# Kernel tuning notes

Measured on AMD Instinct MI355X. Metric: run time of the kernel, lower is better.

## Reference

```python
import jax, jax.numpy as jnp
import numpy as np

B, M, D = 2048, 40, 64          # batch, num fields, embedding dim
HIDDEN = [128, 128, 128]        # CIN layer sizes


def setup_inputs() -> dict:
    key = jax.random.key(0)
    kx, k0, k1, k2 = jax.random.split(key, 4)
    x = jax.random.normal(kx, (B, M, D), dtype=jnp.float32)
    # torch.rand -> uniform [0, 1)
    W0 = jax.random.uniform(k0, (M, M, HIDDEN[0]), dtype=jnp.float32)
    W1 = jax.random.uniform(k1, (M, HIDDEN[0], HIDDEN[1]), dtype=jnp.float32)
    W2 = jax.random.uniform(k2, (M, HIDDEN[1], HIDDEN[2]), dtype=jnp.float32)
    return {"x": x, "W0": W0, "W1": W1, "W2": W2}


def _cin_forward(x, Ws):
    # x: [b, m, d]. Each layer k:
    #   x_next[b, l, d] = sum_{m, h} x0[b, m, d] * x_k[b, h, d] * W_k[m, h, l]
    # which equals the torch 'bil,bjl->bjil' outer product followed by
    # 'bijk,ijl->bkl' + transpose, but expressed as one fused contraction
    # (opt_einsum picks a path avoiding the worst intermediate).
    ps = []
    xk = x  # [b, H_k, d], H_0 = m
    for W in Ws:
        x_next = jnp.einsum('bmd,bhd,mhl->bld', x, xk, W)  # [b, L_k, d]
        ps.append(jnp.sum(x_next, axis=2))                  # [b, L_k]
        xk = x_next
    return jnp.concatenate(ps, axis=1)                      # [b, sum(L_k)]


def reference(x, W0, W1, W2):
    return _cin_forward(x, (W0, W1, W2))
```

## Files before the change

### kernel.cpp

```cpp
#include <hip/hip_runtime.h>
#include <hip/hip_bf16.h>
#include <cstdint>

#define BATCH 2048
#define MF    40
#define DDIM  64
#define LDIM  128
#define ROWS  (BATCH * DDIM)

typedef __attribute__((ext_vector_type(4)))  short    short4_t;
typedef __attribute__((ext_vector_type(8)))  short    short8;
typedef __attribute__((ext_vector_type(8)))  __bf16   bf16x8;
typedef __attribute__((ext_vector_type(2)))  float    floatx2;
typedef __attribute__((ext_vector_type(16))) float    floatx16;

__device__ __forceinline__ unsigned short f32_to_bf16(float f) {
    union { float f; uint32_t u; } v; v.f = f;
    uint32_t u = v.u;
    uint32_t r = (u + 0x7fffu + ((u >> 16) & 1u)) >> 16;
    return (unsigned short)r;
}

__device__ __forceinline__ void barrier_raw() {
    asm volatile("s_barrier" ::: "memory");
}
__device__ __forceinline__ void lgkmwait0() {
    asm volatile("s_waitcnt lgkmcnt(0)" ::: "memory");
}
template <int N> __device__ __forceinline__ void vmwait() {
    if constexpr (N == 0)  asm volatile("s_waitcnt vmcnt(0)"  ::: "memory");
    if constexpr (N == 4)  asm volatile("s_waitcnt vmcnt(4)"  ::: "memory");
    if constexpr (N == 6)  asm volatile("s_waitcnt vmcnt(6)"  ::: "memory");
    if constexpr (N == 10) asm volatile("s_waitcnt vmcnt(10)" ::: "memory");
}

__global__ void k_wprep_all(const float* __restrict__ W0, const float* __restrict__ W1,
                            const float* __restrict__ W2,
                            unsigned short* __restrict__ W0t,
                            unsigned short* __restrict__ W1t,
                            unsigned short* __restrict__ W2t) {
    int bi = blockIdx.x;
    const float* W; unsigned short* Wt; int KK, H;
    if (bi < 640)       { W = W0; Wt = W0t; KK = 4; H = 40; }
    else if (bi < 1920) { bi -= 640;  W = W1; Wt = W1t; KK = 8; H = 128; }
    else                { bi -= 1920; W = W2; Wt = W2t; KK = 8; H = 128; }
    int lane = threadIdx.x;
    int cb = bi & 3;
    int mkk = bi >> 2;
    int kk = mkk % KK, m = mkk / KK;
    int l = cb * 32 + (lane & 31);
    int hbase = kk * 16 + (lane >> 5) * 8;
    unsigned short o[8];
#pragma unroll
    for (int j = 0; j < 8; ++j) {
        int h = hbase + j;
        float v = (h < H) ? W[((size_t)m * H + h) * LDIM + l] : 0.f;
        o[j] = f32_to_bf16(v);
    }
    *(short8*)(Wt + (((size_t)(m * KK + kk) * 4 + cb) * 64 + lane) * 8) = *(const short8*)o;
}

template <int KK>
__device__ __forceinline__ void layer_loop(
    const unsigned short* __restrict__ Wt,
    const float* __restrict__ x, int b,
    int lane, int hf, int r31, int cbg0, int cbg1,
    unsigned short* slabf,
    bf16x8 (&xk)[2][8], floatx16 (&acc)[2][2])
{
    constexpr int UPM  = KK / 4;
    constexpr int NU   = MF * UPM;
    constexpr int GATE = (KK == 8) ? 10 : 6;

    auto stage = [&](int uu) {
        int u = uu < NU ? uu : NU - 1;
        const unsigned short* src = Wt + (size_t)u * 8192;
        const int tid = threadIdx.x;
#pragma unroll
        for (int it = 0; it < 4; ++it) {
            int c = it * 256 + tid;
            __builtin_amdgcn_global_load_lds(
                (const __attribute__((address_space(1))) uint32_t*)(src + (size_t)c * 8),
                (__attribute__((address_space(3))) uint32_t*)(&slabf[(size_t)(u & 3) * 8192 + (size_t)c * 8]),
                16, 0, 0);
        }
    };
    auto ldfrag = [&](int u, int frag, int cb) {
        return __builtin_bit_cast(bf16x8, *(const short8*)(
            &slabf[(size_t)(u & 3) * 8192 + ((size_t)(frag * 4 + cb) * 64 + lane) * 8]));
    };

    acc[0][0] = floatx16{}; acc[0][1] = floatx16{};
    acc[1][0] = floatx16{}; acc[1][1] = floatx16{};

    vmwait<0>();
    stage(0); stage(1); stage(2);
    vmwait<4>();
    barrier_raw();

    bf16x8 bbuf[2][2];
#pragma unroll
    for (int p = 0; p < 2; ++p) {
        bbuf[p][0] = ldfrag(0, p, cbg0);
        bbuf[p][1] = ldfrag(0, p, cbg1);
    }

    float s0v = 0.f, s1v = 0.f;

#pragma unroll 1
    for (int m = 0; m < MF; ++m) {
        floatx16 P[2][2] = {};
#pragma unroll
        for (int kk = 0; kk < KK; ++kk) {
            if (kk % 4 == 0) {
                barrier_raw();
                asm volatile("s_setprio 1");
                if (kk == 0) {
                    const float* sp = x + ((size_t)b * MF + m) * DDIM + r31;
                    s0v = sp[0];
                    s1v = sp[32];
                }
                stage(m * UPM + kk / 4 + 3);
            }
            const int slot = kk & 1;
            P[0][0] = __builtin_amdgcn_mfma_f32_32x32x16_bf16(bbuf[slot][0], xk[0][kk], P[0][0], 0, 0, 0);
            P[1][0] = __builtin_amdgcn_mfma_f32_32x32x16_bf16(bbuf[slot][0], xk[1][kk], P[1][0], 0, 0, 0);
            P[0][1] = __builtin_amdgcn_mfma_f32_32x32x16_bf16(bbuf[slot][1], xk[0][kk], P[0][1], 0, 0, 0);
            P[1][1] = __builtin_amdgcn_mfma_f32_32x32x16_bf16(bbuf[slot][1], xk[1][kk], P[1][1], 0, 0, 0);
            {
                const int j  = kk + 2;
                int mm = m + ((j >= KK) ? 1 : 0);
                if (mm > MF - 1) mm = MF - 1;
                const int jj = (j >= KK) ? (j - KK) : j;
                const int u  = mm * UPM + jj / 4;
                bbuf[slot][0] = ldfrag(u, jj % 4, cbg0);
                bbuf[slot][1] = ldfrag(u, jj % 4, cbg1);
            }
            if (kk % 4 == 3) vmwait<GATE>();
        }
        asm volatile("s_setprio 0");
#pragma unroll
        for (int t = 0; t < 2; ++t) {
            const float sv = (t == 0) ? s0v : s1v;
            floatx2 s2 = {sv, sv};
#pragma unroll
            for (int cbp = 0; cbp < 2; ++cbp) {
                floatx2*       A = (floatx2*)&acc[t][cbp];
                const floatx2* Q = (const floatx2*)&P[t][cbp];
#pragma unroll
                for (int i = 0; i < 8; ++i) A[i] += s2 * Q[i];
            }
        }
    }
}

__global__ __launch_bounds__(256, 2) void k_cin(
    const float* __restrict__ x,
    const unsigned short* __restrict__ W0t,
    const unsigned short* __restrict__ W1t,
    const unsigned short* __restrict__ W2t,
    float* __restrict__ out)
{
    __shared__ unsigned short slab[4][8192];
    unsigned short* slabf = &slab[0][0];

    const int tid  = threadIdx.x;
    const int lane = tid & 63, wave = tid >> 6;
    const int hf   = lane >> 5, r31 = lane & 31;
    const int rowhalf = wave >> 1, colhalf = wave & 1;
    const int b = blockIdx.x * 2 + rowhalf;
    const int cbg0 = colhalf * 2, cbg1 = colhalf * 2 + 1;

    bf16x8   xk[2][8];
    floatx16 acc[2][2];

    auto write_ps = [&](int OFF) {
#pragma unroll
        for (int cbp = 0; cbp < 2; ++cbp) {
#pragma unroll
            for (int j = 0; j < 16; ++j) {
                float v = acc[0][cbp][j] + acc[1][cbp][j];
                v += __shfl_xor(v, 16);
                v += __shfl_xor(v, 8);
                v += __shfl_xor(v, 4);
                v += __shfl_xor(v, 2);
                v += __shfl_xor(v, 1);
                if (r31 == 0)
                    out[(size_t)b * 384 + OFF + (colhalf * 2 + cbp) * 32 +
                        (j & 3) + 8 * (j >> 2) + 4 * hf] = v;
            }
        }
    };

    auto exchange = [&]() {
        vmwait<0>();
        barrier_raw();
#pragma unroll
        for (int t = 0; t < 2; ++t)
#pragma unroll
            for (int cbp = 0; cbp < 2; ++cbp)
#pragma unroll
                for (int g = 0; g < 4; ++g) {
                    unsigned short o[4];
#pragma unroll
                    for (int i = 0; i < 4; ++i) o[i] = f32_to_bf16(acc[t][cbp][g * 4 + i]);
                    const int kk  = colhalf * 4 + cbp * 2 + (g >> 1);
                    const int hfr = g & 1;
                    *(short4_t*)(&slabf[(size_t)rowhalf * 8192 +
                        ((size_t)(t * 8 + kk) * 64 + hfr * 32 + r31) * 8 + 4 * hf]) =
                        *(const short4_t*)o;
                }
        lgkmwait0();
        barrier_raw();
#pragma unroll
        for (int t = 0; t < 2; ++t)
#pragma unroll
            for (int kk = 0; kk < 8; ++kk)
                xk[t][kk] = __builtin_bit_cast(bf16x8, *(const short8*)(
                    &slabf[(size_t)rowhalf * 8192 + ((size_t)(t * 8 + kk) * 64 + lane) * 8]));
        lgkmwait0();
        barrier_raw();
    };

#pragma unroll
    for (int t = 0; t < 2; ++t)
#pragma unroll
        for (int kk = 0; kk < 4; ++kk) {
            unsigned short tmp[8];
#pragma unroll
            for (int j = 0; j < 8; ++j) {
                int h = kk * 16 + hf * 8 + j;
                float v = (h < MF) ? x[((size_t)b * MF + h) * DDIM + t * 32 + r31] : 0.f;
                tmp[j] = f32_to_bf16(v);
            }
            xk[t][kk] = __builtin_bit_cast(bf16x8, *(const short8*)tmp);
        }

    layer_loop<4>(W0t, x, b, lane, hf, r31, cbg0, cbg1, slabf, xk, acc);
    write_ps(0);
    exchange();

    layer_loop<8>(W1t, x, b, lane, hf, r31, cbg0, cbg1, slabf, xk, acc);
    write_ps(128);
    exchange();

    layer_loop<8>(W2t, x, b, lane, hf, r31, cbg0, cbg1, slabf, xk, acc);
    write_ps(256);
}

extern "C" void kernel_launch(void* const* d_in, const int* in_sizes, int n_in,
                              void* d_out, int out_size, void* d_ws, size_t ws_size,
                              hipStream_t stream) {
    const float* x  = (const float*)d_in[0];
    const float* W0 = (const float*)d_in[1];
    const float* W1 = (const float*)d_in[2];
    const float* W2 = (const float*)d_in[3];
    float* out = (float*)d_out;

    char* ws = (char*)d_ws;
    size_t off = 0;
    auto alloc = [&](size_t bytes) -> void* {
        void* p = ws + off;
        off += (bytes + 255) & ~(size_t)255;
        return p;
    };
    unsigned short* W0t = (unsigned short*)alloc((size_t)MF * 4 * 2048 * 2);
    unsigned short* W1t = (unsigned short*)alloc((size_t)MF * 8 * 2048 * 2);
    unsigned short* W2t = (unsigned short*)alloc((size_t)MF * 8 * 2048 * 2);

    k_wprep_all<<<3200, 64, 0, stream>>>(W0, W1, W2, W0t, W1t, W2t);
    k_cin<<<ROWS / 128, 256, 0, stream>>>(x, W0t, W1t, W2t, out);
}
```

Baseline: 434.1 us.

## Prefetch x scalars one field ahead, zero MFMA init via register, stagger blocks

Loads the per-field x scalars one iteration early so the global load latency is hidden behind the MFMA loop. The MFMA accumulator is zeroed by feeding a zero vector built once in registers on kk==0, replacing the per-iteration zero-initialisation of P. The weight conversion kernel now uses nontemporal loads. Every other group of 256 blocks sleeps briefly at start, presumably to stagger memory traffic. The sleep adds idle time and the prefetch holds extra registers.

```diff
diff --git a/kernel.cpp b/kernel.cpp
--- a/kernel.cpp
+++ b/kernel.cpp
@@ -13,6 +13,7 @@
 typedef __attribute__((ext_vector_type(8)))  __bf16   bf16x8;
 typedef __attribute__((ext_vector_type(2)))  float    floatx2;
 typedef __attribute__((ext_vector_type(16))) float    floatx16;
+
 
 __device__ __forceinline__ unsigned short f32_to_bf16(float f) {
     union { float f; uint32_t u; } v; v.f = f;
@@ -54,7 +55,7 @@
 #pragma unroll
     for (int j = 0; j < 8; ++j) {
         int h = hbase + j;
-        float v = (h < H) ? W[((size_t)m * H + h) * LDIM + l] : 0.f;
+        float v = (h < H) ? __builtin_nontemporal_load(&W[((size_t)m * H + h) * LDIM + l]) : 0.f;
         o[j] = f32_to_bf16(v);
     }
     *(short8*)(Wt + (((size_t)(m * KK + kk) * 4 + cb) * 64 + lane) * 8) = *(const short8*)o;
@@ -93,7 +94,19 @@
     acc[0][0] = floatx16{}; acc[0][1] = floatx16{};
     acc[1][0] = floatx16{}; acc[1][1] = floatx16{};
 
+    float z0;
+    asm("v_mov_b32 %0, 0" : "=v"(z0));
+    floatx16 zc;
+#pragma unroll
+    for (int i = 0; i < 16; ++i) zc[i] = z0;
+
     vmwait<0>();
+    float s0n, s1n;
+    {
+        const float* sp = x + ((size_t)b * MF + 0) * DDIM + r31;
+        s0n = sp[0];
+        s1n = sp[32];
+    }
     stage(0); stage(1); stage(2);
     vmwait<4>();
     barrier_raw();
@@ -109,24 +122,26 @@
 
 #pragma unroll 1
     for (int m = 0; m < MF; ++m) {
-        floatx16 P[2][2] = {};
+        floatx16 P[2][2];
 #pragma unroll
         for (int kk = 0; kk < KK; ++kk) {
             if (kk % 4 == 0) {
                 barrier_raw();
                 asm volatile("s_setprio 1");
                 if (kk == 0) {
-                    const float* sp = x + ((size_t)b * MF + m) * DDIM + r31;
-                    s0v = sp[0];
-                    s1v = sp[32];
+                    s0v = s0n; s1v = s1n;
+                    const int mn = (m + 1 < MF) ? m + 1 : MF - 1;
+                    const float* sp = x + ((size_t)b * MF + mn) * DDIM + r31;
+                    s0n = sp[0];
+                    s1n = sp[32];
                 }
                 stage(m * UPM + kk / 4 + 3);
             }
             const int slot = kk & 1;
-            P[0][0] = __builtin_amdgcn_mfma_f32_32x32x16_bf16(bbuf[slot][0], xk[0][kk], P[0][0], 0, 0, 0);
-            P[1][0] = __builtin_amdgcn_mfma_f32_32x32x16_bf16(bbuf[slot][0], xk[1][kk], P[1][0], 0, 0, 0);
-            P[0][1] = __builtin_amdgcn_mfma_f32_32x32x16_bf16(bbuf[slot][1], xk[0][kk], P[0][1], 0, 0, 0);
-            P[1][1] = __builtin_amdgcn_mfma_f32_32x32x16_bf16(bbuf[slot][1], xk[1][kk], P[1][1], 0, 0, 0);
+            P[0][0] = __builtin_amdgcn_mfma_f32_32x32x16_bf16(bbuf[slot][0], xk[0][kk], (kk == 0) ? zc : P[0][0], 0, 0, 0);
+            P[1][0] = __builtin_amdgcn_mfma_f32_32x32x16_bf16(bbuf[slot][0], xk[1][kk], (kk == 0) ? zc : P[1][0], 0, 0, 0);
+            P[0][1] = __builtin_amdgcn_mfma_f32_32x32x16_bf16(bbuf[slot][1], xk[0][kk], (kk == 0) ? zc : P[0][1], 0, 0, 0);
+            P[1][1] = __builtin_amdgcn_mfma_f32_32x32x16_bf16(bbuf[slot][1], xk[1][kk], (kk == 0) ? zc : P[1][1], 0, 0, 0);
             {
                 const int j  = kk + 2;
                 int mm = m + ((j >= KK) ? 1 : 0);
@@ -163,6 +178,10 @@
 {
     __shared__ unsigned short slab[4][8192];
     unsigned short* slabf = &slab[0][0];
+
+    if ((blockIdx.x >> 8) & 1) {
+        asm volatile("s_sleep 15");
+    }
 
     const int tid  = threadIdx.x;
     const int lane = tid & 63, wave = tid >> 6;
```

Result: no change. 434.3 us (+0.0%).
